# Optimization experiments

Measured on AMD Instinct MI355X. Metric: run time of the kernel, lower is better.

Reference implementation:

```python
import jax, jax.numpy as jnp
import numpy as np

B = 4      # cfg.TRAIN.IMS_PER_BATCH
P = 256    # proposals per image (equal per image; all labels > 0)
C = 151    # cfg.MODEL.NUM_CLASSES
R = 51     # cfg.MODEL.NUM_RELATIONS
W = 0.5    # cfg.REL_INFER.NONE_BGREL_WEIGHT


def setup_inputs() -> dict:
    key = jax.random.key(0)
    k1, k2, k3, k4 = jax.random.split(key, 4)
    roi_scores = jax.random.normal(k1, (B * P, C), dtype=jnp.float32)
    rel_scores = jax.random.normal(k2, (B * P * P, R), dtype=jnp.float32)
    roi_labels = jax.random.randint(k3, (B * P,), 1, C, dtype=jnp.int32)  # labels > 0 (fg only)
    # sparse relation co-occurrence matrix densified; background relation slice set to 1
    relationship_mat = (jax.random.uniform(k4, (C, C, R)) < 0.05).astype(jnp.float32)
    relationship_mat = relationship_mat.at[:, :, 0].set(1.0)
    return {
        "roi_scores": roi_scores,
        "rel_scores": rel_scores,
        "relationship_mat": relationship_mat,
        "roi_labels": roi_labels,
        "num_images": B,
    }


def reference(roi_scores, rel_scores, relationship_mat, roi_labels, num_images):
    nb = num_images
    p = roi_scores.shape[0] // nb
    rel = rel_scores.reshape(nb, p, p, -1)          # [B, P, P, R]
    labels = roi_labels.reshape(nb, p)              # [B, P]
    # computed in the original forward but unused by the returned loss
    _unary = jax.nn.log_softmax(roi_scores, axis=1)
    off_diag = (1.0 - jnp.eye(p, dtype=roi_scores.dtype))  # zero out p == q pairs

    def per_image(lab, rl):
        # lab: [P] int, rl: [P, P, R]
        A = relationship_mat[lab]        # [P, C, R]  rows gathered by subject label
        At = relationship_mat[:, lab]    # [C, P, R]  cols gathered by subject label
        # b[p,q,c] = A[p,c,0]*rl[p,q,0] + W * sum_{r>=1} A[p,c,r]*rl[p,q,r]
        b = A[:, None, :, 0] * rl[:, :, None, 0] \
            + W * jnp.einsum('pcr,pqr->pqc', A[..., 1:], rl[..., 1:])
        # t[p,q,c] = At[c,p,0]*rl[q,p,0] + W * sum_{r>=1} At[c,p,r]*rl[q,p,r]
        t = At[..., 0].T[:, None, :] * rl[..., 0].T[:, :, None] \
            + W * jnp.einsum('cpr,qpr->pqc', At[..., 1:], rl[..., 1:])
        theta = 0.5 * (b + t) * off_diag[:, :, None]  # mask diagonal pairs
        theta = theta.sum(0)                          # sum over partner p -> [P, C]
        logp = jax.nn.log_softmax(theta, axis=1)
        return -logp[jnp.arange(p), lab]              # [P]

    loss = jax.vmap(per_image)(labels, rel)           # [B, P]
    return loss.mean()
```

## Files before the change

### kernel.cpp

```cpp
#include <hip/hip_runtime.h>
#include <math.h>

#define NB 4
#define PP 256
#define CC 151
#define RR 51
#define CM 160
#define KS 64
#define NROW (NB*PP)
#define RELTOT (NB*PP*PP*RR)
#define ALIM (RELTOT - 8)
#define MLB 10240
#define TILE 5120

typedef _Float16 half8 __attribute__((ext_vector_type(8)));
typedef float floatx16 __attribute__((ext_vector_type(16)));

#define OFF_M1 ((size_t)0)
#define OFF_M2 (OFF_M1 + (size_t)CC*MLB*2)
#define OFF_PT (OFF_M2 + (size_t)CC*MLB*2)

__global__ __launch_bounds__(256) void prep_kernel(const float* __restrict__ M,
                                                   _Float16* __restrict__ m1,
                                                   _Float16* __restrict__ m2,
                                                   float* __restrict__ out) {
    const int l = blockIdx.x;
    const int mat = blockIdx.y;
    if (l == 0 && mat == 0 && threadIdx.x == 0) *out = 0.f;
    _Float16* dst = (mat ? m2 : m1) + (size_t)l * MLB;
    for (int e = threadIdx.x; e < MLB; e += 256) {
        int oct = e / 1280;
        int rem = e - oct * 1280;
        int c = rem >> 3, j = rem & 7;
        int r = oct * 8 + j;
        float v = 0.f;
        if (r < RR && c < CC) {
            size_t src = ((size_t)(mat ? c * CC + l : l * CC + c)) * RR + r;
            v = (r == 0 ? 0.5f : 0.25f) * M[src];
        }
        dst[e] = (_Float16)v;
    }
}

__global__ __launch_bounds__(256, 2) void gemm_kernel(const float* __restrict__ rel,
                                                      const _Float16* __restrict__ m1,
                                                      const _Float16* __restrict__ m2,
                                                      const int* __restrict__ labels,
                                                      float* __restrict__ part) {
    __shared__ _Float16 Bt[3][TILE];
    const int tid  = threadIdx.x;
    const int ks   = blockIdx.x & 63;
    const int rbk  = (blockIdx.x >> 6) & 1;
    const int n    = blockIdx.x >> 7;
    const int wave = tid >> 6, lane = tid & 63;
    const int m32  = lane & 31, kh = lane >> 5;
    const int i0   = ks * 4;
    const int rowimg = rbk * 128 + wave * 32 + m32;

    int labs[4];
    #pragma unroll
    for (int j = 0; j < 4; ++j) labs[j] = labels[n * PP + i0 + j];

    floatx16 acc[5];
    #pragma unroll
    for (int ct = 0; ct < 5; ++ct)
        #pragma unroll
        for (int r2 = 0; r2 < 16; ++r2) acc[ct][r2] = 0.f;

    auto stageB = [&](int h, int buf) {
        const int il = h >> 2, t = h & 3;
        const size_t moff = (size_t)labs[il] * MLB + t * 2560;
        const _Float16* b1 = m1 + moff;
        const _Float16* b2 = m2 + moff;
        #pragma unroll
        for (int j = 0; j < 3; ++j) {
            int s = j * 256 + tid;
            if (s < 640) {
                const _Float16* g = (s < 320) ? b1 + (size_t)s * 8
                                              : b2 + (size_t)(s - 320) * 8;
                __builtin_amdgcn_global_load_lds(
                    (const __attribute__((address_space(1))) unsigned int*)g,
                    (__attribute__((address_space(3))) unsigned int*)(&Bt[buf][(size_t)s * 8]),
                    16, 0, 0);
            }
        }
    };
    auto loadA = [&](int h, float* v) {
        const int il = h >> 2, t = h & 3;
        const int i = i0 + il;
        const int r0 = t * 16 + kh * 8;
        int idx0 = ((n * PP + i) * PP + rowimg) * RR + r0;
        int idx1 = ((n * PP + rowimg) * PP + i) * RR + r0;
        idx0 = min(idx0, ALIM);
        idx1 = min(idx1, ALIM);
        const float* p0 = rel + idx0;
        const float* p1 = rel + idx1;
        #pragma unroll
        for (int j = 0; j < 8; ++j) { v[j] = p0[j]; v[8 + j] = p1[j]; }
    };

    stageB(0, 0);
    stageB(1, 1);
    float av[16];
    loadA(0, av);

    for (int h = 0; h < 16; ++h) {
        __syncthreads();
        if (h < 14) stageB(h + 2, (h + 2) % 3);
        float avn[16];
        if (h < 15) loadA(h + 1, avn);

        const bool dz = (i0 + (h >> 2)) == rowimg;
        half8 a0, a1;
        #pragma unroll
        for (int j = 0; j < 8; ++j) {
            a0[j] = (_Float16)(dz ? 0.f : av[j]);
            a1[j] = (_Float16)(dz ? 0.f : av[8 + j]);
        }

        const _Float16* bb = &Bt[h % 3][(size_t)(kh * 160 + m32) * 8];
        #pragma unroll
        for (int ct = 0; ct < 5; ++ct) {
            half8 b0 = *(const half8*)(bb + ct * 256);
            half8 b1 = *(const half8*)(bb + 2560 + ct * 256);
            acc[ct] = __builtin_amdgcn_mfma_f32_32x32x16_f16(a0, b0, acc[ct], 0, 0, 0);
            acc[ct] = __builtin_amdgcn_mfma_f32_32x32x16_f16(a1, b1, acc[ct], 0, 0, 0);
        }
        #pragma unroll
        for (int j = 0; j < 16; ++j) av[j] = avn[j];
    }

    float* pb = part + ((size_t)ks * NROW + n * PP + rbk * 128 + wave * 32) * CM;
    #pragma unroll
    for (int ct = 0; ct < 5; ++ct)
        #pragma unroll
        for (int reg = 0; reg < 16; ++reg) {
            int row = (reg & 3) + 8 * (reg >> 2) + 4 * kh;
            pb[(size_t)row * CM + ct * 32 + m32] = acc[ct][reg];
        }
}

__global__ __launch_bounds__(256) void reduce_loss_kernel(const float* __restrict__ part,
                                                          const int* __restrict__ labels,
                                                          float* __restrict__ out) {
    __shared__ float th[CM];
    const int row = blockIdx.x;
    const int t = threadIdx.x;
    if (t < CM) {
        float s = 0.f;
        #pragma unroll
        for (int ks = 0; ks < KS; ++ks)
            s += part[((size_t)ks * NROW + row) * CM + t];
        th[t] = s;
    }
    __syncthreads();
    if (t < 64) {
        float v0 = (t < CC)       ? th[t]       : -INFINITY;
        float v1 = (t + 64 < CC)  ? th[t + 64]  : -INFINITY;
        float v2 = (t + 128 < CC) ? th[t + 128] : -INFINITY;
        float m = fmaxf(v0, fmaxf(v1, v2));
        #pragma unroll
        for (int o = 32; o > 0; o >>= 1) m = fmaxf(m, __shfl_xor(m, o, 64));
        float s = 0.f;
        if (t < CC)       s += expf(v0 - m);
        if (t + 64 < CC)  s += expf(v1 - m);
        if (t + 128 < CC) s += expf(v2 - m);
        #pragma unroll
        for (int o = 32; o > 0; o >>= 1) s += __shfl_xor(s, o, 64);
        if (t == 0) {
            atomicAdd(out, (m + logf(s) - th[labels[row]]) * (1.0f / NROW));
        }
    }
}

extern "C" void kernel_launch(void* const* d_in, const int* in_sizes, int n_in,
                              void* d_out, int out_size, void* d_ws, size_t ws_size,
                              hipStream_t stream) {
    const float* rel    = (const float*)d_in[1];
    const float* relmat = (const float*)d_in[2];
    const int*   labels = (const int*)d_in[3];
    float* out = (float*)d_out;
    char* ws = (char*)d_ws;

    _Float16* m1 = (_Float16*)(ws + OFF_M1);
    _Float16* m2 = (_Float16*)(ws + OFF_M2);
    float*  part = (float*)(ws + OFF_PT);

    prep_kernel<<<dim3(CC, 2), 256, 0, stream>>>(relmat, m1, m2, out);
    gemm_kernel<<<NB * 2 * KS, 256, 0, stream>>>(rel, m1, m2, labels, part);
    reduce_loss_kernel<<<NROW, 256, 0, stream>>>(part, labels, out);
}
```

Measured before the change: 169.4 us.

## Stage relation A-operand through LDS with vectorized loads and fp16 packing

The A operand (relation scores) was previously loaded per MFMA step with scalar strided loads, clamped at the end of the buffer. It is now loaded once per partner index with 16-byte vector loads, two threads per row. Each load covers the whole 51-wide relation vector, which is scaled by the diagonal mask, packed to fp16 and written into a shared-memory tile that the MFMA loop reads from. The aim is more coalesced global traffic and fewer load instructions per step. The cost is extra LDS space, extra barriers, and a register-held prefetch buffer.

```diff
diff --git a/kernel.cpp b/kernel.cpp
--- a/kernel.cpp
+++ b/kernel.cpp
@@ -8,8 +8,6 @@
 #define CM 160
 #define KS 64
 #define NROW (NB*PP)
-#define RELTOT (NB*PP*PP*RR)
-#define ALIM (RELTOT - 8)
 #define MLB 10240
 #define TILE 5120
 
@@ -19,6 +17,12 @@
 #define OFF_M1 ((size_t)0)
 #define OFF_M2 (OFF_M1 + (size_t)CC*MLB*2)
 #define OFF_PT (OFF_M2 + (size_t)CC*MLB*2)
+
+__device__ __forceinline__ unsigned pk2(float a, float b) {
+    union { _Float16 h[2]; unsigned u; } x;
+    x.h[0] = (_Float16)a; x.h[1] = (_Float16)b;
+    return x.u;
+}
 
 __global__ __launch_bounds__(256) void prep_kernel(const float* __restrict__ M,
                                                    _Float16* __restrict__ m1,
@@ -47,6 +51,7 @@
                                                       const _Float16* __restrict__ m2,
                                                       const int* __restrict__ labels,
                                                       float* __restrict__ part) {
+    __shared__ uint4 Ah[2][8][128];
     __shared__ _Float16 Bt[3][TILE];
     const int tid  = threadIdx.x;
     const int ks   = blockIdx.x & 63;
@@ -55,11 +60,22 @@
     const int wave = tid >> 6, lane = tid & 63;
     const int m32  = lane & 31, kh = lane >> 5;
     const int i0   = ks * 4;
-    const int rowimg = rbk * 128 + wave * 32 + m32;
+    const int q0   = rbk * 128;
+    const int qloc = tid >> 1;
+    const int rg   = tid & 1;
+    const int qglob = q0 + qloc;
 
     int labs[4];
     #pragma unroll
     for (int j = 0; j < 4; ++j) labs[j] = labels[n * PP + i0 + j];
+
+    if (rg == 1) {
+        #pragma unroll
+        for (int m = 0; m < 2; ++m) {
+            ((uint2*)&Ah[m][6][qloc])[1] = (uint2){0u, 0u};
+            Ah[m][7][qloc] = (uint4){0u, 0u, 0u, 0u};
+        }
+    }
 
     floatx16 acc[5];
     #pragma unroll
@@ -85,49 +101,87 @@
             }
         }
     };
-    auto loadA = [&](int h, float* v) {
-        const int il = h >> 2, t = h & 3;
+
+    float4 xa[8], xb[8];
+    float ta[3], tb[3];
+
+    auto issueA = [&](int il) {
         const int i = i0 + il;
-        const int r0 = t * 16 + kh * 8;
-        int idx0 = ((n * PP + i) * PP + rowimg) * RR + r0;
-        int idx1 = ((n * PP + rowimg) * PP + i) * RR + r0;
-        idx0 = min(idx0, ALIM);
-        idx1 = min(idx1, ALIM);
-        const float* p0 = rel + idx0;
-        const float* p1 = rel + idx1;
-        #pragma unroll
-        for (int j = 0; j < 8; ++j) { v[j] = p0[j]; v[8 + j] = p1[j]; }
+        const float* s0 = rel + ((size_t)(n * PP + i) * PP + qglob) * RR + rg * 32;
+        const float* s1 = rel + ((size_t)(n * PP + qglob) * PP + i) * RR + rg * 32;
+        if (rg == 0) {
+            #pragma unroll
+            for (int j = 0; j < 8; ++j) {
+                __builtin_memcpy(&xa[j], s0 + j * 4, 16);
+                __builtin_memcpy(&xb[j], s1 + j * 4, 16);
+            }
+        } else {
+            #pragma unroll
+            for (int j = 0; j < 4; ++j) {
+                __builtin_memcpy(&xa[j], s0 + j * 4, 16);
+                __builtin_memcpy(&xb[j], s1 + j * 4, 16);
+            }
+            #pragma unroll
+            for (int j = 0; j < 3; ++j) { ta[j] = s0[16 + j]; tb[j] = s1[16 + j]; }
+        }
     };
 
-    stageB(0, 0);
-    stageB(1, 1);
-    float av[16];
-    loadA(0, av);
-
-    for (int h = 0; h < 16; ++h) {
-        __syncthreads();
-        if (h < 14) stageB(h + 2, (h + 2) % 3);
-        float avn[16];
-        if (h < 15) loadA(h + 1, avn);
-
-        const bool dz = (i0 + (h >> 2)) == rowimg;
-        half8 a0, a1;
-        #pragma unroll
-        for (int j = 0; j < 8; ++j) {
-            a0[j] = (_Float16)(dz ? 0.f : av[j]);
-            a1[j] = (_Float16)(dz ? 0.f : av[8 + j]);
-        }
-
-        const _Float16* bb = &Bt[h % 3][(size_t)(kh * 160 + m32) * 8];
-        #pragma unroll
-        for (int ct = 0; ct < 5; ++ct) {
-            half8 b0 = *(const half8*)(bb + ct * 256);
-            half8 b1 = *(const half8*)(bb + 2560 + ct * 256);
-            acc[ct] = __builtin_amdgcn_mfma_f32_32x32x16_f16(a0, b0, acc[ct], 0, 0, 0);
-            acc[ct] = __builtin_amdgcn_mfma_f32_32x32x16_f16(a1, b1, acc[ct], 0, 0, 0);
-        }
-        #pragma unroll
-        for (int j = 0; j < 16; ++j) av[j] = avn[j];
+    auto writeA = [&](int il) {
+        const float z = ((i0 + il) == qglob) ? 0.f : 1.f;
+        #pragma unroll
+        for (int m = 0; m < 2; ++m) {
+            const float4* xs = m ? xb : xa;
+            const float*  ts = m ? tb : ta;
+            if (rg == 0) {
+                #pragma unroll
+                for (int ch = 0; ch < 4; ++ch) {
+                    float4 u = xs[2 * ch], v = xs[2 * ch + 1];
+                    uint4 w;
+                    w.x = pk2(z * u.x, z * u.y); w.y = pk2(z * u.z, z * u.w);
+                    w.z = pk2(z * v.x, z * v.y); w.w = pk2(z * v.z, z * v.w);
+                    Ah[m][ch][qloc] = w;
+                }
+            } else {
+                #pragma unroll
+                for (int ch = 0; ch < 2; ++ch) {
+                    float4 u = xs[2 * ch], v = xs[2 * ch + 1];
+                    uint4 w;
+                    w.x = pk2(z * u.x, z * u.y); w.y = pk2(z * u.z, z * u.w);
+                    w.z = pk2(z * v.x, z * v.y); w.w = pk2(z * v.z, z * v.w);
+                    Ah[m][4 + ch][qloc] = w;
+                }
+                uint2 w6;
+                w6.x = pk2(z * ts[0], z * ts[1]);
+                w6.y = pk2(z * ts[2], 0.f);
+                ((uint2*)&Ah[m][6][qloc])[0] = w6;
+            }
+        }
+    };
+
+    issueA(0);
+    stageB(0, 0); stageB(1, 1);
+
+    for (int il = 0; il < 4; ++il) {
+        if (il > 0) __syncthreads();
+        writeA(il);
+        if (il < 3) issueA(il + 1);
+        #pragma unroll
+        for (int t = 0; t < 4; ++t) {
+            const int h = il * 4 + t;
+            __syncthreads();
+            if (h + 2 < 16) stageB(h + 2, (h + 2) % 3);
+
+            half8 a0 = *(const half8*)&Ah[0][t * 2 + kh][wave * 32 + m32];
+            half8 a1 = *(const half8*)&Ah[1][t * 2 + kh][wave * 32 + m32];
+            const _Float16* bb = &Bt[h % 3][(size_t)(kh * 160 + m32) * 8];
+            #pragma unroll
+            for (int ct = 0; ct < 5; ++ct) {
+                half8 b0 = *(const half8*)(bb + ct * 256);
+                half8 b1 = *(const half8*)(bb + 2560 + ct * 256);
+                acc[ct] = __builtin_amdgcn_mfma_f32_32x32x16_f16(a0, b0, acc[ct], 0, 0, 0);
+                acc[ct] = __builtin_amdgcn_mfma_f32_32x32x16_f16(a1, b1, acc[ct], 0, 0, 0);
+            }
+        }
     }
 
     float* pb = part + ((size_t)ks * NROW + n * PP + rbk * 128 + wave * 32) * CM;
```

Result: no change. 170.1 us (+0.4%).
